# Kernel tuning notes

Measured on AMD Instinct MI355X. Metric: run time of the kernel, lower is better.

Reference implementation:

```python
import jax, jax.numpy as jnp
import numpy as np

B, S, D = 16, 2048, 64
SCALE = 1.0 / np.sqrt(np.float32(D))  # forward divides by sqrt(embedding_dim=64)


def setup_inputs() -> dict:
    key = jax.random.key(0)
    ks = jax.random.split(key, 7)
    return {
        "x": jax.random.normal(ks[0], (B, S, D), dtype=jnp.float32),
        "Wq": jax.random.normal(ks[1], (D, D), dtype=jnp.float32) * 0.02,
        "bq": jax.random.normal(ks[2], (D,), dtype=jnp.float32) * 0.02,
        "Wk": jax.random.normal(ks[3], (D, D), dtype=jnp.float32) * 0.02,
        "bk": jax.random.normal(ks[4], (D,), dtype=jnp.float32) * 0.02,
        "Wv": jax.random.normal(ks[5], (D, D), dtype=jnp.float32) * 0.02,
        "bv": jax.random.normal(ks[6], (D,), dtype=jnp.float32) * 0.02,
    }


def reference(x, Wq, bq, Wk, bk, Wv, bv):
    # Linear projections (weights stored [in, out], math-equivalent to nn.Linear)
    q = jnp.einsum("bsd,de->bse", x, Wq) + bq
    k = jnp.einsum("bsd,de->bse", x, Wk) + bk
    v = jnp.einsum("bsd,de->bse", x, Wv) + bv
    # Unfused scores: [B, S, S]
    scores = jnp.einsum("bqd,bkd->bqk", q, k) * jnp.float32(SCALE)
    causal = jnp.tril(jnp.ones((S, S), dtype=bool))  # mask[:S,:S]
    scores = jnp.where(causal, scores, jnp.float32(-jnp.inf))
    attn = jax.nn.softmax(scores, axis=-1)
    # dropout is identity in eval mode (reference baseline)
    out = jnp.einsum("bqk,bkd->bqd", attn, v)
    return out
```

## Files before the change

### kernel.cpp

```cpp
#include <hip/hip_runtime.h>
#include <hip/hip_bf16.h>

#define NB 16
#define SS 2048
#define DD 64

typedef __attribute__((ext_vector_type(8))) short short8;
typedef __attribute__((ext_vector_type(4))) float f32x4;

#define SCL2E 0.18033688011112042f

__device__ __forceinline__ short f2bf(float f) {
  union { float f; unsigned u; } v; v.f = f;
  unsigned r = (v.u + 0x7fffu + ((v.u >> 16) & 1u)) >> 16;
  return (short)r;
}

__device__ __forceinline__ short8 load_a_frag_f32(const float* p) {
  float4 u = *(const float4*)p;
  float4 w = *(const float4*)(p + 4);
  short8 r;
  r[0] = f2bf(u.x); r[1] = f2bf(u.y); r[2] = f2bf(u.z); r[3] = f2bf(u.w);
  r[4] = f2bf(w.x); r[5] = f2bf(w.y); r[6] = f2bf(w.z); r[7] = f2bf(w.w);
  return r;
}

__global__ __launch_bounds__(256) void proj_kernel(
    const float* __restrict__ x,
    const float* __restrict__ Wq, const float* __restrict__ bq,
    const float* __restrict__ Wk, const float* __restrict__ bk,
    const float* __restrict__ Wv, const float* __restrict__ bv,
    ushort* __restrict__ qo, ushort* __restrict__ ko, ushort* __restrict__ vT)
{
  __shared__ __align__(16) ushort Wt[3][64][72];
  __shared__ __align__(16) ushort Vs[64][68];
  const int t = threadIdx.x;
  {
    const float* Ws[3] = {Wq, Wk, Wv};
    for (int m = 0; m < 3; ++m)
      for (int i = 0; i < 4; ++i) {
        int idx = i * 1024 + t * 4;
        int kk = idx >> 6, n0 = idx & 63;
        float4 w4 = *(const float4*)(Ws[m] + kk * 64 + n0);
        Wt[m][n0 + 0][kk] = (ushort)f2bf(w4.x);
        Wt[m][n0 + 1][kk] = (ushort)f2bf(w4.y);
        Wt[m][n0 + 2][kk] = (ushort)f2bf(w4.z);
        Wt[m][n0 + 3][kk] = (ushort)f2bf(w4.w);
      }
  }
  __syncthreads();

  const int lane = t & 63, w = t >> 6;
  const int l15 = lane & 15, quad = lane >> 4;
  const int g = blockIdx.x * 64 + w * 16 + l15;
  short8 a0 = load_a_frag_f32(x + (size_t)g * 64 + quad * 8);
  short8 a1 = load_a_frag_f32(x + (size_t)g * 64 + 32 + quad * 8);
  const int lrow0 = w * 16 + quad * 4;
  const int row0 = blockIdx.x * 64 + lrow0;

  for (int m = 0; m < 3; ++m) {
    const float* bp = (m == 0 ? bq : (m == 1 ? bk : bv));
    for (int nt = 0; nt < 4; ++nt) {
      short8 b0 = *(const short8*)&Wt[m][nt * 16 + l15][quad * 8];
      short8 b1 = *(const short8*)&Wt[m][nt * 16 + l15][32 + quad * 8];
      f32x4 acc = {0.f, 0.f, 0.f, 0.f};
      acc = __builtin_amdgcn_mfma_f32_16x16x32_bf16(a0, b0, acc, 0, 0, 0);
      acc = __builtin_amdgcn_mfma_f32_16x16x32_bf16(a1, b1, acc, 0, 0, 0);
      float bb = bp[nt * 16 + l15];
      if (m == 0) {
        for (int r = 0; r < 4; ++r)
          qo[(size_t)(row0 + r) * 64 + nt * 16 + l15] = (ushort)f2bf(acc[r] + bb);
      } else if (m == 1) {
        for (int r = 0; r < 4; ++r)
          ko[(size_t)(row0 + r) * 64 + nt * 16 + l15] = (ushort)f2bf(acc[r] + bb);
      } else {
        for (int r = 0; r < 4; ++r)
          Vs[lrow0 + r][nt * 16 + l15] = (ushort)f2bf(acc[r] + bb);
      }
    }
  }
  __syncthreads();
  {
    const int batch = blockIdx.x >> 5;
    const int s0 = (blockIdx.x & 31) * 64;
    const int d = t >> 2, j0 = (t & 3) * 16;
    ushort tmp[16];
    for (int j = 0; j < 16; ++j) tmp[j] = Vs[j0 + j][d];
    ushort* dst = vT + (size_t)batch * DD * SS + (size_t)d * SS + s0 + j0;
    ((int4*)dst)[0] = ((int4*)tmp)[0];
    ((int4*)dst)[1] = ((int4*)tmp)[1];
  }
}

template<bool MASKED>
__device__ __forceinline__ void attn_half(
    const f32x4 (&c)[4], float (&l_part)[4], f32x4 (&acc)[4],
    const short8 (&vf0)[4], const short8 (&vf1)[4],
    ushort* __restrict__ Pw, int kb4, int rowb, int l15, int quad)
{
#pragma unroll
  for (int r = 0; r < 4; ++r) {
    float pe[4];
#pragma unroll
    for (int ct = 0; ct < 4; ++ct) {
      pe[ct] = __builtin_amdgcn_exp2f(c[ct][r] * SCL2E);
      if (MASKED && (kb4 + ct > rowb + r)) pe[ct] = 0.f;
    }
    l_part[r] += (pe[0] + pe[1]) + (pe[2] + pe[3]);
    __hip_bfloat162 h01 = __float22bfloat162_rn(make_float2(pe[0], pe[1]));
    __hip_bfloat162 h23 = __float22bfloat162_rn(make_float2(pe[2], pe[3]));
    uint2 pwv;
    pwv.x = *reinterpret_cast<unsigned*>(&h01);
    pwv.y = *reinterpret_cast<unsigned*>(&h23);
    *(uint2*)&Pw[(quad * 4 + r) * 72 + 4 * l15] = pwv;
  }
  short8 pa0 = *(const short8*)&Pw[l15 * 72 + quad * 8];
  short8 pa1 = *(const short8*)&Pw[l15 * 72 + 32 + quad * 8];
#pragma unroll
  for (int nt = 0; nt < 4; ++nt) {
    acc[nt] = __builtin_amdgcn_mfma_f32_16x16x32_bf16(pa0, vf0[nt], acc[nt], 0, 0, 0);
    acc[nt] = __builtin_amdgcn_mfma_f32_16x16x32_bf16(pa1, vf1[nt], acc[nt], 0, 0, 0);
  }
}

__global__ __launch_bounds__(256, 2) void attn_kernel(
    const ushort* __restrict__ qg, const ushort* __restrict__ kg,
    const ushort* __restrict__ vT, float* __restrict__ out)
{
  __shared__ __align__(16) float accW[4][32][68];
  __shared__ float lW[4][32];
  ushort* Pw_base = (ushort*)&accW[0][0][0];

  const int t = threadIdx.x, bid = blockIdx.x;
  const int batch = (bid & 7) * 2 + ((bid >> 3) & 1);
  const int qt = 63 - (bid >> 4);
  const int q0 = qt * 32;
  const int lane = t & 63, w = t >> 6;
  const int l15 = lane & 15, quad = lane >> 4;
  const size_t bbase = (size_t)batch * SS * DD;
  ushort* Pw = Pw_base + w * (16 * 72);

  const ushort* qp = qg + bbase + (size_t)(q0 + l15) * 64 + quad * 8;
  short8 a0 = *(const short8*)qp;
  short8 a1 = *(const short8*)(qp + 32);
  short8 a2 = *(const short8*)(qp + 16 * 64);
  short8 a3 = *(const short8*)(qp + 16 * 64 + 32);

  f32x4 acc0[4], acc1[4];
  float l0[4] = {0.f, 0.f, 0.f, 0.f}, l1[4] = {0.f, 0.f, 0.f, 0.f};
#pragma unroll
  for (int nt = 0; nt < 4; ++nt) {
    acc0[nt] = (f32x4){0.f, 0.f, 0.f, 0.f};
    acc1[nt] = (f32x4){0.f, 0.f, 0.f, 0.f};
  }

  const int ktotal = ((q0 + 31) >> 6) + 1;
  const ushort* kpc = kg + bbase + (size_t)(4 * l15) * 64 + quad * 8
                    + (size_t)(w << 6) * 64;
  const ushort* vp0 = vT + bbase + (size_t)l15 * SS + w * 64 + quad * 8;
  const ushort* vp1 = vp0 + 16 * SS;
  const ushort* vp2 = vp0 + 32 * SS;
  const ushort* vp3 = vp0 + 48 * SS;

  short8 kc0[4], kc1[4];
#pragma unroll
  for (int ct = 0; ct < 4; ++ct) {
    kc0[ct] = *(const short8*)(kpc + ct * 64);
    kc1[ct] = *(const short8*)(kpc + ct * 64 + 32);
  }

  for (int kt = w; kt < ktotal; kt += 4) {
    short8 vf0[4], vf1[4];
    vf0[0] = *(const short8*)(vp0); vf1[0] = *(const short8*)(vp0 + 32);
    vf0[1] = *(const short8*)(vp1); vf1[1] = *(const short8*)(vp1 + 32);
    vf0[2] = *(const short8*)(vp2); vf1[2] = *(const short8*)(vp2 + 32);
    vf0[3] = *(const short8*)(vp3); vf1[3] = *(const short8*)(vp3 + 32);

    const ushort* kpn = (kt + 4 < ktotal) ? (kpc + 16384) : kpc;
    short8 kn0[4], kn1[4];
#pragma unroll
    for (int ct = 0; ct < 4; ++ct) {
      kn0[ct] = *(const short8*)(kpn + ct * 64);
      kn1[ct] = *(const short8*)(kpn + ct * 64 + 32);
    }

    f32x4 c0[4], c1[4];
#pragma unroll
    for (int ct = 0; ct < 4; ++ct) {
      c0[ct] = (f32x4){0.f, 0.f, 0.f, 0.f};
      c0[ct] = __builtin_amdgcn_mfma_f32_16x16x32_bf16(a0, kc0[ct], c0[ct], 0, 0, 0);
      c0[ct] = __builtin_amdgcn_mfma_f32_16x16x32_bf16(a1, kc1[ct], c0[ct], 0, 0, 0);
      c1[ct] = (f32x4){0.f, 0.f, 0.f, 0.f};
      c1[ct] = __builtin_amdgcn_mfma_f32_16x16x32_bf16(a2, kc0[ct], c1[ct], 0, 0, 0);
      c1[ct] = __builtin_amdgcn_mfma_f32_16x16x32_bf16(a3, kc1[ct], c1[ct], 0, 0, 0);
    }

    const int kb4 = kt * 64 + 4 * l15;
    if (kt == ktotal - 1) {
      attn_half<true >(c0, l0, acc0, vf0, vf1, Pw, kb4, q0 + quad * 4, l15, quad);
      attn_half<true >(c1, l1, acc1, vf0, vf1, Pw, kb4, q0 + 16 + quad * 4, l15, quad);
    } else {
      attn_half<false>(c0, l0, acc0, vf0, vf1, Pw, kb4, q0 + quad * 4, l15, quad);
      attn_half<false>(c1, l1, acc1, vf0, vf1, Pw, kb4, q0 + 16 + quad * 4, l15, quad);
    }

#pragma unroll
    for (int ct = 0; ct < 4; ++ct) { kc0[ct] = kn0[ct]; kc1[ct] = kn1[ct]; }
    kpc = kpn;
    vp0 += 256; vp1 += 256; vp2 += 256; vp3 += 256;
  }

#pragma unroll
  for (int r = 0; r < 4; ++r)
    for (int off = 1; off < 16; off <<= 1) {
      l0[r] += __shfl_xor(l0[r], off, 64);
      l1[r] += __shfl_xor(l1[r], off, 64);
    }

  __syncthreads();
#pragma unroll
  for (int r = 0; r < 4; ++r)
#pragma unroll
    for (int nt = 0; nt < 4; ++nt) {
      accW[w][quad * 4 + r][nt * 16 + l15] = acc0[nt][r];
      accW[w][16 + quad * 4 + r][nt * 16 + l15] = acc1[nt][r];
    }
  if (l15 == 0)
#pragma unroll
    for (int r = 0; r < 4; ++r) {
      lW[w][quad * 4 + r] = l0[r];
      lW[w][16 + quad * 4 + r] = l1[r];
    }
  __syncthreads();

  {
    const int row = t >> 3, col0 = (t & 7) * 8;
    float den = lW[0][row] + lW[1][row] + lW[2][row] + lW[3][row];
    float iv = 1.0f / den;
    float4 oa = {0.f, 0.f, 0.f, 0.f}, ob = {0.f, 0.f, 0.f, 0.f};
#pragma unroll
    for (int ww = 0; ww < 4; ++ww) {
      float4 x0 = *(const float4*)&accW[ww][row][col0];
      float4 x1 = *(const float4*)&accW[ww][row][col0 + 4];
      oa.x += x0.x; oa.y += x0.y; oa.z += x0.z; oa.w += x0.w;
      ob.x += x1.x; ob.y += x1.y; ob.z += x1.z; ob.w += x1.w;
    }
    oa.x *= iv; oa.y *= iv; oa.z *= iv; oa.w *= iv;
    ob.x *= iv; ob.y *= iv; ob.z *= iv; ob.w *= iv;
    float* op = out + bbase + (size_t)(q0 + row) * 64 + col0;
    *(float4*)op = oa;
    *(float4*)(op + 4) = ob;
  }
}

extern "C" void kernel_launch(void* const* d_in, const int* in_sizes, int n_in,
                              void* d_out, int out_size, void* d_ws, size_t ws_size,
                              hipStream_t stream) {
  (void)in_sizes; (void)n_in; (void)out_size; (void)ws_size;
  const float* x  = (const float*)d_in[0];
  const float* Wq = (const float*)d_in[1];
  const float* bq = (const float*)d_in[2];
  const float* Wk = (const float*)d_in[3];
  const float* bk = (const float*)d_in[4];
  const float* Wv = (const float*)d_in[5];
  const float* bv = (const float*)d_in[6];
  float* out = (float*)d_out;

  ushort* qws = (ushort*)d_ws;
  ushort* kws = qws + (size_t)NB * SS * DD;
  ushort* vws = kws + (size_t)NB * SS * DD;

  proj_kernel<<<dim3(NB * SS / 64), dim3(256), 0, stream>>>(
      x, Wq, bq, Wk, bk, Wv, bv, qws, kws, vws);
  attn_kernel<<<dim3(NB * (SS / 32)), dim3(256), 0, stream>>>(
      qws, kws, vws, out);
}
```

Before: 118.6 us.

## Split long causal query tiles across key chunks and add combine kernel

The attention kernel now splits each query tile's causal key range into chunks of up to 8 key tiles, giving later query tiles up to 4 blocks. Each block writes partial unnormalized outputs and row sums to a workspace, and a new combine kernel sums the chunks and normalizes. This targets load imbalance from causal triangular work and the tail of long blocks. The cost is an extra kernel launch and workspace traffic. The projection kernel also stages Q and K through shared memory so global writes are coalesced.

```diff
diff --git a/kernel.cpp b/kernel.cpp
--- a/kernel.cpp
+++ b/kernel.cpp
@@ -9,6 +9,8 @@
 typedef __attribute__((ext_vector_type(4))) float f32x4;
 
 #define SCL2E 0.18033688011112042f
+
+#define PSLOT 2080
 
 __device__ __forceinline__ short f2bf(float f) {
   union { float f; unsigned u; } v; v.f = f;
@@ -33,7 +35,7 @@
     ushort* __restrict__ qo, ushort* __restrict__ ko, ushort* __restrict__ vT)
 {
   __shared__ __align__(16) ushort Wt[3][64][72];
-  __shared__ __align__(16) ushort Vs[64][68];
+  __shared__ __align__(16) ushort Vs[64][72];
   const int t = threadIdx.x;
   {
     const float* Ws[3] = {Wq, Wk, Wv};
@@ -56,10 +58,10 @@
   short8 a0 = load_a_frag_f32(x + (size_t)g * 64 + quad * 8);
   short8 a1 = load_a_frag_f32(x + (size_t)g * 64 + 32 + quad * 8);
   const int lrow0 = w * 16 + quad * 4;
-  const int row0 = blockIdx.x * 64 + lrow0;
 
   for (int m = 0; m < 3; ++m) {
     const float* bp = (m == 0 ? bq : (m == 1 ? bk : bv));
+#pragma unroll
     for (int nt = 0; nt < 4; ++nt) {
       short8 b0 = *(const short8*)&Wt[m][nt * 16 + l15][quad * 8];
       short8 b1 = *(const short8*)&Wt[m][nt * 16 + l15][32 + quad * 8];
@@ -67,28 +69,30 @@
       acc = __builtin_amdgcn_mfma_f32_16x16x32_bf16(a0, b0, acc, 0, 0, 0);
       acc = __builtin_amdgcn_mfma_f32_16x16x32_bf16(a1, b1, acc, 0, 0, 0);
       float bb = bp[nt * 16 + l15];
-      if (m == 0) {
-        for (int r = 0; r < 4; ++r)
-          qo[(size_t)(row0 + r) * 64 + nt * 16 + l15] = (ushort)f2bf(acc[r] + bb);
-      } else if (m == 1) {
-        for (int r = 0; r < 4; ++r)
-          ko[(size_t)(row0 + r) * 64 + nt * 16 + l15] = (ushort)f2bf(acc[r] + bb);
-      } else {
-        for (int r = 0; r < 4; ++r)
-          Vs[lrow0 + r][nt * 16 + l15] = (ushort)f2bf(acc[r] + bb);
-      }
-    }
-  }
-  __syncthreads();
-  {
-    const int batch = blockIdx.x >> 5;
-    const int s0 = (blockIdx.x & 31) * 64;
-    const int d = t >> 2, j0 = (t & 3) * 16;
-    ushort tmp[16];
-    for (int j = 0; j < 16; ++j) tmp[j] = Vs[j0 + j][d];
-    ushort* dst = vT + (size_t)batch * DD * SS + (size_t)d * SS + s0 + j0;
-    ((int4*)dst)[0] = ((int4*)tmp)[0];
-    ((int4*)dst)[1] = ((int4*)tmp)[1];
+#pragma unroll
+      for (int r = 0; r < 4; ++r)
+        Vs[lrow0 + r][nt * 16 + l15] = (ushort)f2bf(acc[r] + bb);
+    }
+    __syncthreads();
+    if (m < 2) {
+      ushort* outp = (m == 0 ? qo : ko);
+      const int row = t >> 2, col0 = (t & 3) * 16;
+      int4 d0 = *(const int4*)&Vs[row][col0];
+      int4 d1 = *(const int4*)&Vs[row][col0 + 8];
+      ushort* dst = outp + (size_t)(blockIdx.x * 64 + row) * 64 + col0;
+      ((int4*)dst)[0] = d0;
+      ((int4*)dst)[1] = d1;
+    } else {
+      const int batch = blockIdx.x >> 5;
+      const int s0 = (blockIdx.x & 31) * 64;
+      const int d = t >> 2, j0 = (t & 3) * 16;
+      ushort tmp[16];
+      for (int j = 0; j < 16; ++j) tmp[j] = Vs[j0 + j][d];
+      ushort* dst = vT + (size_t)batch * DD * SS + (size_t)d * SS + s0 + j0;
+      ((int4*)dst)[0] = ((int4*)tmp)[0];
+      ((int4*)dst)[1] = ((int4*)tmp)[1];
+    }
+    if (m < 2) __syncthreads();
   }
 }
 
@@ -123,9 +127,9 @@
   }
 }
 
-__global__ __launch_bounds__(256, 2) void attn_kernel(
+__global__ __launch_bounds__(256, 2) void attn_part(
     const ushort* __restrict__ qg, const ushort* __restrict__ kg,
-    const ushort* __restrict__ vT, float* __restrict__ out)
+    const ushort* __restrict__ vT, float* __restrict__ pws)
 {
   __shared__ __align__(16) float accW[4][32][68];
   __shared__ float lW[4][32];
@@ -133,8 +137,16 @@
 
   const int t = threadIdx.x, bid = blockIdx.x;
   const int batch = (bid & 7) * 2 + ((bid >> 3) & 1);
-  const int qt = 63 - (bid >> 4);
+  const int local = bid >> 4;
+  int qt, c;
+  if (local < 16)      { qt = local;                 c = 0; }
+  else if (local < 48) { int u = local - 16; qt = 16 + (u >> 1); c = u & 1; }
+  else if (local < 96) { int u = local - 48; int q3 = u / 3; qt = 32 + q3; c = u - 3 * q3; }
+  else                 { int u = local - 96; qt = 48 + (u >> 2); c = u & 3; }
+
   const int q0 = qt * 32;
+  const int nkt = (qt >> 1) + 1;
+  const int tend = min(8 * c + 8, nkt);
   const int lane = t & 63, w = t >> 6;
   const int l15 = lane & 15, quad = lane >> 4;
   const size_t bbase = (size_t)batch * SS * DD;
@@ -154,10 +166,10 @@
     acc1[nt] = (f32x4){0.f, 0.f, 0.f, 0.f};
   }
 
-  const int ktotal = ((q0 + 31) >> 6) + 1;
+  const int t0 = 8 * c + w;
   const ushort* kpc = kg + bbase + (size_t)(4 * l15) * 64 + quad * 8
-                    + (size_t)(w << 6) * 64;
-  const ushort* vp0 = vT + bbase + (size_t)l15 * SS + w * 64 + quad * 8;
+                    + (size_t)t0 * 4096;
+  const ushort* vp0 = vT + bbase + (size_t)l15 * SS + t0 * 64 + quad * 8;
   const ushort* vp1 = vp0 + 16 * SS;
   const ushort* vp2 = vp0 + 32 * SS;
   const ushort* vp3 = vp0 + 48 * SS;
@@ -169,14 +181,14 @@
     kc1[ct] = *(const short8*)(kpc + ct * 64 + 32);
   }
 
-  for (int kt = w; kt < ktotal; kt += 4) {
+  for (int kt = t0; kt < tend; kt += 4) {
     short8 vf0[4], vf1[4];
     vf0[0] = *(const short8*)(vp0); vf1[0] = *(const short8*)(vp0 + 32);
     vf0[1] = *(const short8*)(vp1); vf1[1] = *(const short8*)(vp1 + 32);
     vf0[2] = *(const short8*)(vp2); vf1[2] = *(const short8*)(vp2 + 32);
     vf0[3] = *(const short8*)(vp3); vf1[3] = *(const short8*)(vp3 + 32);
 
-    const ushort* kpn = (kt + 4 < ktotal) ? (kpc + 16384) : kpc;
+    const ushort* kpn = (kt + 4 < tend) ? (kpc + 16384) : kpc;
     short8 kn0[4], kn1[4];
 #pragma unroll
     for (int ct = 0; ct < 4; ++ct) {
@@ -196,7 +208,7 @@
     }
 
     const int kb4 = kt * 64 + 4 * l15;
-    if (kt == ktotal - 1) {
+    if (kt == nkt - 1) {
       attn_half<true >(c0, l0, acc0, vf0, vf1, Pw, kb4, q0 + quad * 4, l15, quad);
       attn_half<true >(c1, l1, acc1, vf0, vf1, Pw, kb4, q0 + 16 + quad * 4, l15, quad);
     } else {
@@ -235,8 +247,7 @@
 
   {
     const int row = t >> 3, col0 = (t & 7) * 8;
-    float den = lW[0][row] + lW[1][row] + lW[2][row] + lW[3][row];
-    float iv = 1.0f / den;
+    float* ps = pws + (size_t)(((batch << 6) + qt) * 4 + c) * PSLOT;
     float4 oa = {0.f, 0.f, 0.f, 0.f}, ob = {0.f, 0.f, 0.f, 0.f};
 #pragma unroll
     for (int ww = 0; ww < 4; ++ww) {
@@ -245,12 +256,44 @@
       oa.x += x0.x; oa.y += x0.y; oa.z += x0.z; oa.w += x0.w;
       ob.x += x1.x; ob.y += x1.y; ob.z += x1.z; ob.w += x1.w;
     }
-    oa.x *= iv; oa.y *= iv; oa.z *= iv; oa.w *= iv;
-    ob.x *= iv; ob.y *= iv; ob.z *= iv; ob.w *= iv;
-    float* op = out + bbase + (size_t)(q0 + row) * 64 + col0;
-    *(float4*)op = oa;
-    *(float4*)(op + 4) = ob;
-  }
+    *(float4*)(ps + row * 64 + col0) = oa;
+    *(float4*)(ps + row * 64 + col0 + 4) = ob;
+    if ((t & 7) == 0)
+      ps[2048 + row] = lW[0][row] + lW[1][row] + lW[2][row] + lW[3][row];
+  }
+}
+
+__global__ __launch_bounds__(256) void combine_kernel(
+    const float* __restrict__ pws, float* __restrict__ out)
+{
+  __shared__ float inv_s[32];
+  const int t = threadIdx.x, bid = blockIdx.x;
+  const int batch = bid >> 6, qt = bid & 63;
+  const int q0 = qt * 32;
+  const int nch = (qt >> 4) + 1;
+  const float* ps0 = pws + (size_t)(((batch << 6) + qt) * 4) * PSLOT;
+
+  if (t < 32) {
+    float d = 0.f;
+    for (int c = 0; c < nch; ++c) d += ps0[c * PSLOT + 2048 + t];
+    inv_s[t] = 1.0f / d;
+  }
+  __syncthreads();
+
+  const int row = t >> 3, col0 = (t & 7) * 8;
+  float4 oa = {0.f, 0.f, 0.f, 0.f}, ob = {0.f, 0.f, 0.f, 0.f};
+  for (int c = 0; c < nch; ++c) {
+    float4 x0 = *(const float4*)(ps0 + c * PSLOT + row * 64 + col0);
+    float4 x1 = *(const float4*)(ps0 + c * PSLOT + row * 64 + col0 + 4);
+    oa.x += x0.x; oa.y += x0.y; oa.z += x0.z; oa.w += x0.w;
+    ob.x += x1.x; ob.y += x1.y; ob.z += x1.z; ob.w += x1.w;
+  }
+  float iv = inv_s[row];
+  oa.x *= iv; oa.y *= iv; oa.z *= iv; oa.w *= iv;
+  ob.x *= iv; ob.y *= iv; ob.z *= iv; ob.w *= iv;
+  float* op = out + (size_t)batch * SS * DD + (size_t)(q0 + row) * 64 + col0;
+  *(float4*)op = oa;
+  *(float4*)(op + 4) = ob;
 }
 
 extern "C" void kernel_launch(void* const* d_in, const int* in_sizes, int n_in,
@@ -269,9 +312,11 @@
   ushort* qws = (ushort*)d_ws;
   ushort* kws = qws + (size_t)NB * SS * DD;
   ushort* vws = kws + (size_t)NB * SS * DD;
+  float* pws = (float*)(vws + (size_t)NB * SS * DD);
 
   proj_kernel<<<dim3(NB * SS / 64), dim3(256), 0, stream>>>(
       x, Wq, bq, Wk, bk, Wv, bv, qws, kws, vws);
-  attn_kernel<<<dim3(NB * (SS / 32)), dim3(256), 0, stream>>>(
-      qws, kws, vws, out);
-}
+  attn_part<<<dim3(NB * 160), dim3(256), 0, stream>>>(
+      qws, kws, vws, pws);
+  combine_kernel<<<dim3(NB * 64), dim3(256), 0, stream>>>(pws, out);
+}
```

Measured after the change: 136.2 us. +14.8%, slower.
